# Performance work log

Hardware: AMD Instinct MI355X
Metric: run time of the kernel (lower is better)

## Reference

```python
import jax, jax.numpy as jnp
import numpy as np

N_GRAPHS = 2048
NODES_PER_GRAPH = 128
M = NODES_PER_GRAPH // 2  # atoms per monomer
N_NODES = N_GRAPHS * NODES_PER_GRAPH
DEG = 4
N_EDGES = N_NODES * DEG
F_IN = 64
D = 128
EPS = 1e-5
SLOPE = 0.01


def leaky(h):
    return jnp.where(h > 0, h, SLOPE * h)


def setup_inputs() -> dict:
    key = jax.random.key(0)
    ks = jax.random.split(key, 24)
    rng = np.random.default_rng(0)
    # intra-graph random edges, degree ~4
    offs = np.repeat(np.arange(N_GRAPHS, dtype=np.int32) * NODES_PER_GRAPH, NODES_PER_GRAPH * DEG)
    src = offs + rng.integers(0, NODES_PER_GRAPH, N_EDGES).astype(np.int32)
    dst = offs + rng.integers(0, NODES_PER_GRAPH, N_EDGES).astype(np.int32)
    edge_index = jnp.asarray(np.stack([src, dst]), dtype=jnp.int32)
    batch_index = jnp.asarray(np.repeat(np.arange(N_GRAPHS, dtype=np.int32), NODES_PER_GRAPH))
    # first half of each graph = monomer A (weight 0.3), second half = monomer B (0.7)
    mw_graph = np.concatenate([np.full(M, 0.3, np.float32), np.full(M, 0.7, np.float32)])
    monomer_weight = jnp.asarray(np.tile(mw_graph, N_GRAPHS)[:, None])
    s = 0.05
    inp = {
        "x": jax.random.normal(ks[0], (N_NODES, F_IN), jnp.float32),
        "monomer_weight": monomer_weight,
        "Wc0s": jax.random.normal(ks[1], (F_IN, D)) * s,
        "Wc0n": jax.random.normal(ks[2], (F_IN, D)) * s,
        "bc0": jnp.zeros((D,)),
        "g0": jnp.ones((D,)), "b0": jnp.zeros((D,)),
        "m0": jax.random.normal(ks[3], (D,)) * s, "v0": jnp.ones((D,)),
        "Wc1s": jax.random.normal(ks[4], (D, D)) * s,
        "Wc1n": jax.random.normal(ks[5], (D, D)) * s,
        "bc1": jnp.zeros((D,)),
        "g1": jnp.ones((D,)), "b1": jnp.zeros((D,)),
        "m1": jax.random.normal(ks[6], (D,)) * s, "v1": jnp.ones((D,)),
        "Wa": jax.random.normal(ks[7], (D, D)) * s, "ba": jnp.zeros((D,)),
        "Wr0": jax.random.normal(ks[8], (D, D)) * s, "br0": jnp.zeros((D,)),
        "Wr1": jax.random.normal(ks[9], (D, D)) * s, "br1": jnp.zeros((D,)),
        "Wout": jax.random.normal(ks[10], (D, 1)) * s, "bout": jnp.zeros((1,)),
        "edge_index": edge_index,
        "batch_index": batch_index,
    }
    return inp


def reference(x, monomer_weight, Wc0s, Wc0n, bc0, g0, b0, m0, v0,
              Wc1s, Wc1n, bc1, g1, b1, m1, v1, Wa, ba,
              Wr0, br0, Wr1, br1, Wout, bout, edge_index, batch_index):
    src, dst = edge_index[0], edge_index[1]
    n = x.shape[0]
    deg = jnp.clip(jax.ops.segment_sum(jnp.ones_like(src, jnp.float32), dst, num_segments=n), 1.0)

    def conv(h, Ws, Wn, b):
        agg = jax.ops.segment_sum(h[src], dst, num_segments=n) / deg[:, None]
        return h @ Ws + agg @ Wn + b

    def bn(h, g, b, rm, rv):
        return (h - rm) * jax.lax.rsqrt(rv + EPS) * g + b

    # conv + BN(eval) + leaky_relu (+ dropout identity in eval)
    h = leaky(bn(conv(x, Wc0s, Wc0n, bc0), g0, b0, m0, v0))
    h = leaky(bn(conv(h, Wc1s, Wc1n, bc1), g1, b1, m1, v1))
    # apply monomer weighting BeforePooling
    h = h * monomer_weight
    # pairwise monomer cross-attention (regular layout: [G, 2M, D])
    hg = h.reshape(N_GRAPHS, NODES_PER_GRAPH, D)
    mA, mB = hg[:, :M], hg[:, M:]
    pA = leaky(mA @ Wa + ba)
    pB = leaky(mB @ Wa + ba)
    pair = jax.nn.sigmoid(jnp.einsum('gmd,gnd->gmn', pA, pB))
    newA = jnp.einsum('gmn,gnd->gmd', pair, pB) + mA
    newB = jnp.einsum('gmn,gmd->gnd', pair, pA) + mB
    h = jnp.concatenate([newA, newB], axis=1).reshape(n, D)
    # scatter-based global mean pool
    pooled = jax.ops.segment_sum(h, batch_index, num_segments=N_GRAPHS)
    cnt = jax.ops.segment_sum(jnp.ones((n,), jnp.float32), batch_index, num_segments=N_GRAPHS)
    pooled = pooled / cnt[:, None]
    # readout MLP (dropout identity in eval)
    r = leaky(pooled @ Wr0 + br0)
    r = leaky(r @ Wr1 + br1)
    return r @ Wout + bout
```

## Files before the change

kernel.cpp:

```cpp
#include <hip/hip_runtime.h>

#define N_EDGES_C 1048576

typedef __attribute__((ext_vector_type(8))) __bf16 bf16x8;
typedef __attribute__((ext_vector_type(4))) __bf16 bf16x4;
typedef __attribute__((ext_vector_type(4))) float f32x4;
typedef __attribute__((ext_vector_type(4))) unsigned int u32x4;

#define MFMA16(a,b,c) __builtin_amdgcn_mfma_f32_16x16x32_bf16((a),(b),(c),0,0,0)

__device__ __forceinline__ unsigned short f2bf(float f) {
  unsigned int u = __builtin_bit_cast(unsigned int, f);
  u = (u + 0x7fffu + ((u >> 16) & 1u)) >> 16;
  return (unsigned short)u;
}
__device__ __forceinline__ float bf2f(unsigned short h) {
  unsigned int u = ((unsigned int)h) << 16;
  return __builtin_bit_cast(float, u);
}

__device__ __forceinline__ bf16x8 fragM(const unsigned short* sM, int row, int kb, int lane) {
  int r = row + (lane & 15);
  int cb = (kb + ((lane >> 4) << 3)) * 2;
  return *(const bf16x8*)((const char*)sM + r * 256 + (cb ^ ((r & 7) << 4)));
}
__device__ __forceinline__ void putBf(unsigned short* sM, int r, int c, float v) {
  *(__bf16*)((char*)sM + r * 256 + ((c * 2) ^ ((r & 7) << 4))) = (__bf16)v;
}
__device__ __forceinline__ bf16x8 adjFrag(const unsigned char* sCc, float inv,
                                          int mBase, int kb, int lane) {
  int m = mBase + (lane & 15);
  int c = (kb + ((lane >> 4) << 3)) ^ ((m & 7) << 3);
  const unsigned int* p = (const unsigned int*)(sCc + m * 128 + c);
  unsigned int w0 = p[0], w1 = p[1];
  bf16x8 r;
#pragma unroll
  for (int i = 0; i < 4; i++) {
    r[i]     = (__bf16)((float)((w0 >> (8 * i)) & 0xffu) * inv);
    r[4 + i] = (__bf16)((float)((w1 >> (8 * i)) & 0xffu) * inv);
  }
  return r;
}

__device__ __forceinline__ u32x4 stG32(const unsigned short* src, int KS, int ko, int t) {
  int row = t >> 2, ks = t & 3;
  return *(const u32x4*)(src + row * KS + ko + ks * 8);
}
__device__ __forceinline__ void stW32(unsigned short* buf, int t, u32x4 v) {
  int row = t >> 2, ks = t & 3;
  int slot = (ks + row + (row >> 2)) & 3;
  *(u32x4*)((char*)buf + row * 64 + slot * 16) = v;
}
__device__ __forceinline__ bf16x8 fragW32(const unsigned short* buf, int nc, int lane) {
  int r = nc + (lane & 15);
  int ks = lane >> 4;
  int slot = (ks + r + (r >> 2)) & 3;
  return *(const bf16x8*)((const char*)buf + r * 64 + slot * 16);
}

__global__ void prep_kernel(const float* __restrict__ Wc0s, const float* __restrict__ Wc0n,
                            const float* __restrict__ Wc1s, const float* __restrict__ Wc1n,
                            const float* __restrict__ Wa,
                            const float* __restrict__ bc0, const float* __restrict__ g0,
                            const float* __restrict__ b0, const float* __restrict__ m0,
                            const float* __restrict__ v0,
                            const float* __restrict__ bc1, const float* __restrict__ g1,
                            const float* __restrict__ b1, const float* __restrict__ m1,
                            const float* __restrict__ v1,
                            const float* __restrict__ Wr0, const float* __restrict__ Wr1,
                            unsigned short* __restrict__ wbf, float* __restrict__ cst,
                            float* __restrict__ wr0t, float* __restrict__ wr1t) {
  int t = blockIdx.x * blockDim.x + threadIdx.x;
  if (t < 8192) {
    int d = t >> 6, f = t & 63;
    wbf[t]        = f2bf(Wc0s[f * 128 + d]);
    wbf[8192 + t] = f2bf(Wc0n[f * 128 + d]);
  } else if (t < 24576) {
    int i = t - 8192;
    int d = i >> 7, k = i & 127;
    wbf[16384 + i] = f2bf(Wc1s[k * 128 + d]);
    wbf[32768 + i] = f2bf(Wc1n[k * 128 + d]);
    wbf[49152 + i] = f2bf(Wa[k * 128 + d]);
  } else if (t < 24704) {
    int d = t - 24576;
    float s0 = g0[d] * rsqrtf(v0[d] + 1e-5f);
    cst[d]       = s0;
    cst[128 + d] = (bc0[d] - m0[d]) * s0 + b0[d];
    float s1 = g1[d] * rsqrtf(v1[d] + 1e-5f);
    cst[256 + d] = s1;
    cst[384 + d] = (bc1[d] - m1[d]) * s1 + b1[d];
  } else if (t < 57472) {
    int i = t - 24704;
    int which = i >> 14;
    int k = i & 16383;
    int d = k >> 7, j = k & 127;
    float v = (which ? Wr1 : Wr0)[j * 128 + d];
    (which ? wr1t : wr0t)[k] = v;
  }
}

__global__ __launch_bounds__(512, 4)
void gnn_fused(const float* __restrict__ x, const float* __restrict__ mwt,
               const int* __restrict__ ei,
               const unsigned short* __restrict__ wbf, const float* __restrict__ cst,
               const float* __restrict__ ba,
               const float* __restrict__ wr0t, const float* __restrict__ br0,
               const float* __restrict__ wr1t, const float* __restrict__ br1,
               const float* __restrict__ Wout, const float* __restrict__ bout,
               float* __restrict__ out) {
  __shared__ unsigned short sM[128 * 128];
  __shared__ unsigned char  sC[128 * 128];
  __shared__ unsigned short sW[3][4096];
  __shared__ float sInv[128];
  __shared__ float sPool[128];
  __shared__ float sV1[128];
  __shared__ float sOut;

  const int g = blockIdx.x;
  const int t = threadIdx.x;
  const int lane = t & 63;
  const int w = t >> 6;
  const int col = lane & 15;
  const int r0 = (lane >> 4) << 2;
  const f32x4 zero = {0.f, 0.f, 0.f, 0.f};
  u32x4 st0, st1;

  st0 = stG32(wbf + 8192, 64, 0, t);
  st1 = stG32(wbf + 8192, 64, 32, t);
  u32x4 st2 = stG32(wbf, 64, 0, t);
  {
    unsigned int* c32 = (unsigned int*)sC;
    for (int i = t; i < 4096; i += 512) c32[i] = 0u;
    if (t < 128) { sPool[t] = 0.f; sV1[t] = 0.f; }
    if (t == 0) sOut = 0.f;
  }
  {
    const float4* xg = (const float4*)(x + (size_t)g * 8192);
#pragma unroll
    for (int i = 0; i < 4; i++) {
      int vi = t + i * 512;
      float4 v = xg[vi];
      int node = vi >> 4;
      int f = (vi & 15) * 4;
      bf16x4 q = {(__bf16)v.x, (__bf16)v.y, (__bf16)v.z, (__bf16)v.w};
      *(bf16x4*)((char*)sM + node * 256 + ((f * 2) ^ ((node & 7) << 4))) = q;
    }
  }
  __syncthreads();

  {
    int e = g * 512 + t;
    int ls_ = ei[e] & 127;
    int ld_ = ei[N_EDGES_C + e] & 127;
    int cb = ls_ ^ ((ld_ & 7) << 3);
    int idx = ld_ * 128 + cb;
    atomicAdd((unsigned int*)(sC + (idx & ~3)), 1u << ((idx & 3) * 8));
  }
  stW32(sW[0], t, st0);
  stW32(sW[1], t, st1);
  stW32(sW[2], t, st2);
  bf16x8 xA0 = fragM(sM, w * 16, 0, lane);
  bf16x8 xA1 = fragM(sM, w * 16, 32, lane);
  __syncthreads();

  f32x4 acc[8];

  {
    int row = t >> 2, q = t & 3;
    const unsigned int* rp = (const unsigned int*)(sC + row * 128) + q * 8;
    int ssum = 0;
#pragma unroll
    for (int i = 0; i < 8; i++) {
      unsigned int v = rp[i];
      ssum += (int)(v & 0xff) + (int)((v >> 8) & 0xff) + (int)((v >> 16) & 0xff) + (int)(v >> 24);
    }
    ssum += __shfl_xor(ssum, 1);
    ssum += __shfl_xor(ssum, 2);
    if (q == 0) sInv[row] = 1.f / (float)(ssum > 1 ? ssum : 1);
  }
  st0 = stG32(wbf, 64, 32, t);
  st1 = stG32(wbf + 32768, 128, 0, t);
#pragma unroll
  for (int n = 0; n < 8; n++) acc[n] = zero;
#pragma unroll
  for (int n = 0; n < 8; n++) acc[n] = MFMA16(xA0, fragW32(sW[0], n * 16, lane), acc[n]);
#pragma unroll
  for (int n = 0; n < 8; n++) acc[n] = MFMA16(xA1, fragW32(sW[1], n * 16, lane), acc[n]);
#pragma unroll
  for (int n = 0; n < 8; n++) {
    bf16x4 q = {(__bf16)acc[n][0], (__bf16)acc[n][1], (__bf16)acc[n][2], (__bf16)acc[n][3]};
    int d = n * 16 + col;
    *(bf16x4*)((char*)sM + d * 256 + (((w * 16 + r0) * 2) ^ ((d & 7) << 4))) = q;
  }
  __syncthreads();

  stW32(sW[0], t, st0);
  stW32(sW[1], t, st1);
  st0 = stG32(wbf + 32768, 128, 32, t);
  const float invRow = sInv[w * 16 + col];
#pragma unroll
  for (int n = 0; n < 8; n++) acc[n] = zero;
#pragma unroll
  for (int n = 0; n < 8; n++) acc[n] = MFMA16(xA0, fragW32(sW[2], n * 16, lane), acc[n]);
  for (int kb = 0; kb < 4; kb++) {
    bf16x8 aF = adjFrag(sC, invRow, w * 16, kb * 32, lane);
#pragma unroll
    for (int n = 0; n < 8; n++)
      acc[n] = MFMA16(aF, fragM(sM, n * 16, kb * 32, lane), acc[n]);
  }
  __syncthreads();

  stW32(sW[2], t, st0);
  st1 = stG32(wbf + 32768, 128, 64, t);
#pragma unroll
  for (int n = 0; n < 8; n++) acc[n] = MFMA16(xA1, fragW32(sW[0], n * 16, lane), acc[n]);
#pragma unroll
  for (int n = 0; n < 8; n++) {
    int d = n * 16 + col;
    float mul = cst[d], add = cst[128 + d];
#pragma unroll
    for (int r = 0; r < 4; r++) {
      float v = acc[n][r] * mul + add;
      v = v > 0.f ? v : 0.01f * v;
      putBf(sM, w * 16 + r0 + r, d, v);
    }
  }
  bf16x8 hA0 = fragM(sM, w * 16, 0, lane);
  bf16x8 hA1 = fragM(sM, w * 16, 32, lane);
  bf16x8 hA2 = fragM(sM, w * 16, 64, lane);
  bf16x8 hA3 = fragM(sM, w * 16, 96, lane);
  __syncthreads();

  stW32(sW[0], t, st1);
  st0 = stG32(wbf + 32768, 128, 96, t);
#pragma unroll
  for (int n = 0; n < 8; n++) acc[n] = zero;
#pragma unroll
  for (int n = 0; n < 8; n++) acc[n] = MFMA16(hA0, fragW32(sW[1], n * 16, lane), acc[n]);
  __syncthreads();

  stW32(sW[1], t, st0);
  st1 = stG32(wbf + 16384, 128, 0, t);
#pragma unroll
  for (int n = 0; n < 8; n++) acc[n] = MFMA16(hA1, fragW32(sW[2], n * 16, lane), acc[n]);
  __syncthreads();

  stW32(sW[2], t, st1);
  st0 = stG32(wbf + 16384, 128, 32, t);
#pragma unroll
  for (int n = 0; n < 8; n++) acc[n] = MFMA16(hA2, fragW32(sW[0], n * 16, lane), acc[n]);
  __syncthreads();

  stW32(sW[0], t, st0);
  st1 = stG32(wbf + 16384, 128, 64, t);
#pragma unroll
  for (int n = 0; n < 8; n++) acc[n] = MFMA16(hA3, fragW32(sW[1], n * 16, lane), acc[n]);
#pragma unroll
  for (int n = 0; n < 8; n++) {
    bf16x4 q = {(__bf16)acc[n][0], (__bf16)acc[n][1], (__bf16)acc[n][2], (__bf16)acc[n][3]};
    int d = n * 16 + col;
    *(bf16x4*)((char*)sM + d * 256 + (((w * 16 + r0) * 2) ^ ((d & 7) << 4))) = q;
  }
  __syncthreads();

  stW32(sW[1], t, st1);
  st0 = stG32(wbf + 16384, 128, 96, t);
#pragma unroll
  for (int n = 0; n < 8; n++) acc[n] = zero;
  for (int kb = 0; kb < 4; kb++) {
    bf16x8 aF = adjFrag(sC, invRow, w * 16, kb * 32, lane);
#pragma unroll
    for (int n = 0; n < 8; n++)
      acc[n] = MFMA16(aF, fragM(sM, n * 16, kb * 32, lane), acc[n]);
  }
  __syncthreads();

  st1 = stG32(wbf + 49152, 128, 0, t);
#pragma unroll
  for (int n = 0; n < 8; n++) acc[n] = MFMA16(hA0, fragW32(sW[2], n * 16, lane), acc[n]);
  __syncthreads();

  stW32(sW[2], t, st0);
  st0 = stG32(wbf + 49152, 128, 32, t);
  float mwr[4];
#pragma unroll
  for (int r = 0; r < 4; r++) mwr[r] = mwt[(size_t)g * 128 + w * 16 + r0 + r];
#pragma unroll
  for (int n = 0; n < 8; n++) acc[n] = MFMA16(hA1, fragW32(sW[0], n * 16, lane), acc[n]);
  __syncthreads();

  stW32(sW[0], t, st1);
  st1 = stG32(wbf + 49152, 128, 64, t);
#pragma unroll
  for (int n = 0; n < 8; n++) acc[n] = MFMA16(hA2, fragW32(sW[1], n * 16, lane), acc[n]);
  __syncthreads();

  stW32(sW[1], t, st0);
  st0 = stG32(wbf + 49152, 128, 96, t);
#pragma unroll
  for (int n = 0; n < 8; n++) acc[n] = MFMA16(hA3, fragW32(sW[2], n * 16, lane), acc[n]);
#pragma unroll
  for (int n = 0; n < 8; n++) {
    int d = n * 16 + col;
    float mul = cst[256 + d], add = cst[384 + d];
    float csum = 0.f;
#pragma unroll
    for (int r = 0; r < 4; r++) {
      float v = acc[n][r] * mul + add;
      v = v > 0.f ? v : 0.01f * v;
      v *= mwr[r];
      putBf(sM, w * 16 + r0 + r, d, v);
      csum += v;
    }
    csum += __shfl_xor(csum, 16);
    csum += __shfl_xor(csum, 32);
    if (lane < 16) atomicAdd(&sPool[d], csum);
  }
  hA0 = fragM(sM, w * 16, 0, lane);
  hA1 = fragM(sM, w * 16, 32, lane);
  hA2 = fragM(sM, w * 16, 64, lane);
  hA3 = fragM(sM, w * 16, 96, lane);
  __syncthreads();

  stW32(sW[2], t, st1);
#pragma unroll
  for (int n = 0; n < 8; n++) acc[n] = zero;
#pragma unroll
  for (int n = 0; n < 8; n++) acc[n] = MFMA16(hA0, fragW32(sW[0], n * 16, lane), acc[n]);
  __syncthreads();

  stW32(sW[0], t, st0);
#pragma unroll
  for (int n = 0; n < 8; n++) acc[n] = MFMA16(hA1, fragW32(sW[1], n * 16, lane), acc[n]);
  __syncthreads();

#pragma unroll
  for (int n = 0; n < 8; n++) acc[n] = MFMA16(hA2, fragW32(sW[2], n * 16, lane), acc[n]);
  __syncthreads();

#pragma unroll
  for (int n = 0; n < 8; n++) acc[n] = MFMA16(hA3, fragW32(sW[0], n * 16, lane), acc[n]);
#pragma unroll
  for (int n = 0; n < 8; n++) {
    int d = n * 16 + col;
    float bav = ba[d];
#pragma unroll
    for (int r = 0; r < 4; r++) {
      float v = acc[n][r] + bav;
      v = v > 0.f ? v : 0.01f * v;
      putBf(sM, w * 16 + r0 + r, d, v);
    }
  }
  __syncthreads();

  {
    f32x4 acc2[2] = {zero, zero};
    for (int kb = 0; kb < 128; kb += 32) {
#pragma unroll
      for (int i = 0; i < 2; i++) {
        int T = w * 2 + i;
        bf16x8 a = fragM(sM, (T >> 2) * 16, kb, lane);
        bf16x8 b = fragM(sM, 64 + (T & 3) * 16, kb, lane);
        acc2[i] = MFMA16(a, b, acc2[i]);
      }
    }
#pragma unroll
    for (int i = 0; i < 2; i++) {
      int T = w * 2 + i, mb = (T >> 2) * 16, nb = (T & 3) * 16;
      float s0 = 1.f / (1.f + __expf(-acc2[i][0]));
      float s1 = 1.f / (1.f + __expf(-acc2[i][1]));
      float s2 = 1.f / (1.f + __expf(-acc2[i][2]));
      float s3 = 1.f / (1.f + __expf(-acc2[i][3]));
      atomicAdd(&sV1[64 + nb + col], s0 + s1 + s2 + s3);
#pragma unroll
      for (int m = 1; m < 16; m <<= 1) {
        s0 += __shfl_xor(s0, m);
        s1 += __shfl_xor(s1, m);
        s2 += __shfl_xor(s2, m);
        s3 += __shfl_xor(s3, m);
      }
      if (col < 4) {
        float v = col == 0 ? s0 : (col == 1 ? s1 : (col == 2 ? s2 : s3));
        atomicAdd(&sV1[mb + r0 + col], v);
      }
    }
  }
  __syncthreads();

  {
    int d = t & 127, q = t >> 7;
    float s = 0.f;
#pragma unroll
    for (int i = 0; i < 32; i++) {
      int node = q * 32 + i;
      float u = sV1[node];
      float pv = bf2f(*(const unsigned short*)((const char*)sM + node * 256 +
                                               ((2 * d) ^ ((node & 7) << 4))));
      s += u * pv;
    }
    atomicAdd(&sPool[d], s);
  }
  __syncthreads();

  if (t < 128) sPool[t] *= (1.f / 128.f);
  __syncthreads();
  {
    int d = t >> 2, q = t & 3;
    const float* row = wr0t + d * 128 + q * 32;
    float s = 0.f;
#pragma unroll
    for (int j = 0; j < 32; j++) s += sPool[q * 32 + j] * row[j];
    s += __shfl_xor(s, 1);
    s += __shfl_xor(s, 2);
    if (q == 0) { s += br0[d]; sV1[d] = s > 0.f ? s : 0.01f * s; }
  }
  __syncthreads();
  {
    int d = t >> 2, q = t & 3;
    const float* row = wr1t + d * 128 + q * 32;
    float s = 0.f;
#pragma unroll
    for (int j = 0; j < 32; j++) s += sV1[q * 32 + j] * row[j];
    s += __shfl_xor(s, 1);
    s += __shfl_xor(s, 2);
    if (q == 0) { s += br1[d]; sPool[d] = s > 0.f ? s : 0.01f * s; }
  }
  __syncthreads();
  if (t < 128) atomicAdd(&sOut, sPool[t] * Wout[t]);
  __syncthreads();
  if (t == 0) out[g] = sOut + bout[0];
}

extern "C" void kernel_launch(void* const* d_in, const int* in_sizes, int n_in,
                              void* d_out, int out_size, void* d_ws, size_t ws_size,
                              hipStream_t stream) {
  const float* x     = (const float*)d_in[0];
  const float* mwt   = (const float*)d_in[1];
  const float* Wc0s  = (const float*)d_in[2];
  const float* Wc0n  = (const float*)d_in[3];
  const float* bc0   = (const float*)d_in[4];
  const float* g0    = (const float*)d_in[5];
  const float* b0    = (const float*)d_in[6];
  const float* m0    = (const float*)d_in[7];
  const float* v0    = (const float*)d_in[8];
  const float* Wc1s  = (const float*)d_in[9];
  const float* Wc1n  = (const float*)d_in[10];
  const float* bc1   = (const float*)d_in[11];
  const float* g1    = (const float*)d_in[12];
  const float* b1    = (const float*)d_in[13];
  const float* m1    = (const float*)d_in[14];
  const float* v1    = (const float*)d_in[15];
  const float* Wa    = (const float*)d_in[16];
  const float* ba    = (const float*)d_in[17];
  const float* Wr0   = (const float*)d_in[18];
  const float* br0   = (const float*)d_in[19];
  const float* Wr1   = (const float*)d_in[20];
  const float* br1   = (const float*)d_in[21];
  const float* Wout  = (const float*)d_in[22];
  const float* bout  = (const float*)d_in[23];
  const int*   ei    = (const int*)d_in[24];

  unsigned short* wbf = (unsigned short*)d_ws;
  float* cst  = (float*)((char*)d_ws + 131072);
  float* wr0t = (float*)((char*)d_ws + 133120);
  float* wr1t = (float*)((char*)d_ws + 198656);

  prep_kernel<<<dim3(225), dim3(256), 0, stream>>>(Wc0s, Wc0n, Wc1s, Wc1n, Wa,
                                                   bc0, g0, b0, m0, v0,
                                                   bc1, g1, b1, m1, v1,
                                                   Wr0, Wr1, wbf, cst, wr0t, wr1t);
  gnn_fused<<<dim3(2048), dim3(512), 0, stream>>>(x, mwt, ei, wbf, cst, ba,
                                                  wr0t, br0, wr1t, br1, Wout, bout,
                                                  (float*)d_out);
}
```

Measured before the change: 161.5 us.

## Use LDS-only barriers, compute degree by atomics, split readout MLP into separate kernel

Every __syncthreads is replaced with a barrier that waits only on LDS counters (lgkmcnt), so global weight prefetches stay in flight across barriers. Edge indices are loaded earlier to overlap with the x load. Node degree is now accumulated with float atomics at edge-insert time, which removes the row-sum pass over the count matrix. The readout MLP moves out of the fused kernel into a second 128-thread kernel that reads pooled vectors from workspace. This adds a launch and a global round trip for the pooled data, and the custom barrier relies on vmcnt ordering being handled elsewhere.

```diff
diff --git a/kernel.cpp b/kernel.cpp
--- a/kernel.cpp
+++ b/kernel.cpp
@@ -8,6 +8,10 @@
 typedef __attribute__((ext_vector_type(4))) unsigned int u32x4;
 
 #define MFMA16(a,b,c) __builtin_amdgcn_mfma_f32_16x16x32_bf16((a),(b),(c),0,0,0)
+
+#define BARRIER() do { asm volatile("s_waitcnt lgkmcnt(0)" ::: "memory"); \
+                       __builtin_amdgcn_s_barrier(); \
+                       asm volatile("" ::: "memory"); } while (0)
 
 __device__ __forceinline__ unsigned short f2bf(float f) {
   unsigned int u = __builtin_bit_cast(unsigned int, f);
@@ -104,19 +108,15 @@
                const int* __restrict__ ei,
                const unsigned short* __restrict__ wbf, const float* __restrict__ cst,
                const float* __restrict__ ba,
-               const float* __restrict__ wr0t, const float* __restrict__ br0,
-               const float* __restrict__ wr1t, const float* __restrict__ br1,
-               const float* __restrict__ Wout, const float* __restrict__ bout,
-               float* __restrict__ out) {
+               float* __restrict__ pooled) {
   __shared__ unsigned short sM[128 * 128];
   __shared__ unsigned char  sC[128 * 128];
   __shared__ unsigned short sW[3][4096];
-  __shared__ float sInv[128];
+  __shared__ float sDeg[128];
   __shared__ float sPool[128];
   __shared__ float sV1[128];
-  __shared__ float sOut;
-
-  const int g = blockIdx.x;
+
+  const int gb = blockIdx.x;
   const int t = threadIdx.x;
   const int lane = t & 63;
   const int w = t >> 6;
@@ -128,14 +128,19 @@
   st0 = stG32(wbf + 8192, 64, 0, t);
   st1 = stG32(wbf + 8192, 64, 32, t);
   u32x4 st2 = stG32(wbf, 64, 0, t);
+  int els, eld;
+  {
+    int e = gb * 512 + t;
+    els = ei[e] & 127;
+    eld = ei[N_EDGES_C + e] & 127;
+  }
   {
     unsigned int* c32 = (unsigned int*)sC;
     for (int i = t; i < 4096; i += 512) c32[i] = 0u;
-    if (t < 128) { sPool[t] = 0.f; sV1[t] = 0.f; }
-    if (t == 0) sOut = 0.f;
-  }
-  {
-    const float4* xg = (const float4*)(x + (size_t)g * 8192);
+    if (t < 128) { sPool[t] = 0.f; sV1[t] = 0.f; sDeg[t] = 0.f; }
+  }
+  {
+    const float4* xg = (const float4*)(x + (size_t)gb * 8192);
 #pragma unroll
     for (int i = 0; i < 4; i++) {
       int vi = t + i * 512;
@@ -146,38 +151,23 @@
       *(bf16x4*)((char*)sM + node * 256 + ((f * 2) ^ ((node & 7) << 4))) = q;
     }
   }
-  __syncthreads();
-
-  {
-    int e = g * 512 + t;
-    int ls_ = ei[e] & 127;
-    int ld_ = ei[N_EDGES_C + e] & 127;
-    int cb = ls_ ^ ((ld_ & 7) << 3);
-    int idx = ld_ * 128 + cb;
+  BARRIER();
+
+  {
+    int cb = els ^ ((eld & 7) << 3);
+    int idx = eld * 128 + cb;
     atomicAdd((unsigned int*)(sC + (idx & ~3)), 1u << ((idx & 3) * 8));
+    atomicAdd(&sDeg[eld], 1.f);
   }
   stW32(sW[0], t, st0);
   stW32(sW[1], t, st1);
   stW32(sW[2], t, st2);
   bf16x8 xA0 = fragM(sM, w * 16, 0, lane);
   bf16x8 xA1 = fragM(sM, w * 16, 32, lane);
-  __syncthreads();
+  BARRIER();
 
   f32x4 acc[8];
 
-  {
-    int row = t >> 2, q = t & 3;
-    const unsigned int* rp = (const unsigned int*)(sC + row * 128) + q * 8;
-    int ssum = 0;
-#pragma unroll
-    for (int i = 0; i < 8; i++) {
-      unsigned int v = rp[i];
-      ssum += (int)(v & 0xff) + (int)((v >> 8) & 0xff) + (int)((v >> 16) & 0xff) + (int)(v >> 24);
-    }
-    ssum += __shfl_xor(ssum, 1);
-    ssum += __shfl_xor(ssum, 2);
-    if (q == 0) sInv[row] = 1.f / (float)(ssum > 1 ? ssum : 1);
-  }
   st0 = stG32(wbf, 64, 32, t);
   st1 = stG32(wbf + 32768, 128, 0, t);
 #pragma unroll
@@ -192,12 +182,12 @@
     int d = n * 16 + col;
     *(bf16x4*)((char*)sM + d * 256 + (((w * 16 + r0) * 2) ^ ((d & 7) << 4))) = q;
   }
-  __syncthreads();
+  BARRIER();
 
   stW32(sW[0], t, st0);
   stW32(sW[1], t, st1);
   st0 = stG32(wbf + 32768, 128, 32, t);
-  const float invRow = sInv[w * 16 + col];
+  const float invRow = 1.f / fmaxf(sDeg[w * 16 + col], 1.f);
 #pragma unroll
   for (int n = 0; n < 8; n++) acc[n] = zero;
 #pragma unroll
@@ -208,7 +198,7 @@
     for (int n = 0; n < 8; n++)
       acc[n] = MFMA16(aF, fragM(sM, n * 16, kb * 32, lane), acc[n]);
   }
-  __syncthreads();
+  BARRIER();
 
   stW32(sW[2], t, st0);
   st1 = stG32(wbf + 32768, 128, 64, t);
@@ -229,7 +219,7 @@
   bf16x8 hA1 = fragM(sM, w * 16, 32, lane);
   bf16x8 hA2 = fragM(sM, w * 16, 64, lane);
   bf16x8 hA3 = fragM(sM, w * 16, 96, lane);
-  __syncthreads();
+  BARRIER();
 
   stW32(sW[0], t, st1);
   st0 = stG32(wbf + 32768, 128, 96, t);
@@ -237,19 +227,19 @@
   for (int n = 0; n < 8; n++) acc[n] = zero;
 #pragma unroll
   for (int n = 0; n < 8; n++) acc[n] = MFMA16(hA0, fragW32(sW[1], n * 16, lane), acc[n]);
-  __syncthreads();
+  BARRIER();
 
   stW32(sW[1], t, st0);
   st1 = stG32(wbf + 16384, 128, 0, t);
 #pragma unroll
   for (int n = 0; n < 8; n++) acc[n] = MFMA16(hA1, fragW32(sW[2], n * 16, lane), acc[n]);
-  __syncthreads();
+  BARRIER();
 
   stW32(sW[2], t, st1);
   st0 = stG32(wbf + 16384, 128, 32, t);
 #pragma unroll
   for (int n = 0; n < 8; n++) acc[n] = MFMA16(hA2, fragW32(sW[0], n * 16, lane), acc[n]);
-  __syncthreads();
+  BARRIER();
 
   stW32(sW[0], t, st0);
   st1 = stG32(wbf + 16384, 128, 64, t);
@@ -261,7 +251,7 @@
     int d = n * 16 + col;
     *(bf16x4*)((char*)sM + d * 256 + (((w * 16 + r0) * 2) ^ ((d & 7) << 4))) = q;
   }
-  __syncthreads();
+  BARRIER();
 
   stW32(sW[1], t, st1);
   st0 = stG32(wbf + 16384, 128, 96, t);
@@ -273,27 +263,27 @@
     for (int n = 0; n < 8; n++)
       acc[n] = MFMA16(aF, fragM(sM, n * 16, kb * 32, lane), acc[n]);
   }
-  __syncthreads();
+  BARRIER();
 
   st1 = stG32(wbf + 49152, 128, 0, t);
 #pragma unroll
   for (int n = 0; n < 8; n++) acc[n] = MFMA16(hA0, fragW32(sW[2], n * 16, lane), acc[n]);
-  __syncthreads();
+  BARRIER();
 
   stW32(sW[2], t, st0);
   st0 = stG32(wbf + 49152, 128, 32, t);
   float mwr[4];
 #pragma unroll
-  for (int r = 0; r < 4; r++) mwr[r] = mwt[(size_t)g * 128 + w * 16 + r0 + r];
+  for (int r = 0; r < 4; r++) mwr[r] = mwt[(size_t)gb * 128 + w * 16 + r0 + r];
 #pragma unroll
   for (int n = 0; n < 8; n++) acc[n] = MFMA16(hA1, fragW32(sW[0], n * 16, lane), acc[n]);
-  __syncthreads();
+  BARRIER();
 
   stW32(sW[0], t, st1);
   st1 = stG32(wbf + 49152, 128, 64, t);
 #pragma unroll
   for (int n = 0; n < 8; n++) acc[n] = MFMA16(hA2, fragW32(sW[1], n * 16, lane), acc[n]);
-  __syncthreads();
+  BARRIER();
 
   stW32(sW[1], t, st0);
   st0 = stG32(wbf + 49152, 128, 96, t);
@@ -320,23 +310,23 @@
   hA1 = fragM(sM, w * 16, 32, lane);
   hA2 = fragM(sM, w * 16, 64, lane);
   hA3 = fragM(sM, w * 16, 96, lane);
-  __syncthreads();
+  BARRIER();
 
   stW32(sW[2], t, st1);
 #pragma unroll
   for (int n = 0; n < 8; n++) acc[n] = zero;
 #pragma unroll
   for (int n = 0; n < 8; n++) acc[n] = MFMA16(hA0, fragW32(sW[0], n * 16, lane), acc[n]);
-  __syncthreads();
+  BARRIER();
 
   stW32(sW[0], t, st0);
 #pragma unroll
   for (int n = 0; n < 8; n++) acc[n] = MFMA16(hA1, fragW32(sW[1], n * 16, lane), acc[n]);
-  __syncthreads();
+  BARRIER();
 
 #pragma unroll
   for (int n = 0; n < 8; n++) acc[n] = MFMA16(hA2, fragW32(sW[2], n * 16, lane), acc[n]);
-  __syncthreads();
+  BARRIER();
 
 #pragma unroll
   for (int n = 0; n < 8; n++) acc[n] = MFMA16(hA3, fragW32(sW[0], n * 16, lane), acc[n]);
@@ -351,7 +341,7 @@
       putBf(sM, w * 16 + r0 + r, d, v);
     }
   }
-  __syncthreads();
+  BARRIER();
 
   {
     f32x4 acc2[2] = {zero, zero};
@@ -385,7 +375,7 @@
       }
     }
   }
-  __syncthreads();
+  BARRIER();
 
   {
     int d = t & 127, q = t >> 7;
@@ -400,35 +390,46 @@
     }
     atomicAdd(&sPool[d], s);
   }
+  BARRIER();
+
+  if (t < 128) pooled[(size_t)gb * 128 + t] = sPool[t] * (1.f / 128.f);
+}
+
+__global__ __launch_bounds__(128)
+void readout_kernel(const float* __restrict__ pooled,
+                    const float* __restrict__ wr0t, const float* __restrict__ br0,
+                    const float* __restrict__ wr1t, const float* __restrict__ br1,
+                    const float* __restrict__ Wout, const float* __restrict__ bout,
+                    float* __restrict__ out) {
+  __shared__ float pl[128], t1[128];
+  __shared__ float sred[2];
+  int g = blockIdx.x, t = threadIdx.x;
+  pl[t] = pooled[(size_t)g * 128 + t];
   __syncthreads();
-
-  if (t < 128) sPool[t] *= (1.f / 128.f);
+  {
+    const float* row = wr0t + t * 128;
+    float s = 0.f;
+#pragma unroll 8
+    for (int j = 0; j < 128; j++) s += pl[j] * row[j];
+    s += br0[t];
+    t1[t] = s > 0.f ? s : 0.01f * s;
+  }
   __syncthreads();
-  {
-    int d = t >> 2, q = t & 3;
-    const float* row = wr0t + d * 128 + q * 32;
+  float v2;
+  {
+    const float* row = wr1t + t * 128;
     float s = 0.f;
-#pragma unroll
-    for (int j = 0; j < 32; j++) s += sPool[q * 32 + j] * row[j];
-    s += __shfl_xor(s, 1);
-    s += __shfl_xor(s, 2);
-    if (q == 0) { s += br0[d]; sV1[d] = s > 0.f ? s : 0.01f * s; }
-  }
+#pragma unroll 8
+    for (int j = 0; j < 128; j++) s += t1[j] * row[j];
+    s += br1[t];
+    s = s > 0.f ? s : 0.01f * s;
+    v2 = s * Wout[t];
+  }
+#pragma unroll
+  for (int m = 1; m < 64; m <<= 1) v2 += __shfl_xor(v2, m);
+  if ((t & 63) == 0) sred[t >> 6] = v2;
   __syncthreads();
-  {
-    int d = t >> 2, q = t & 3;
-    const float* row = wr1t + d * 128 + q * 32;
-    float s = 0.f;
-#pragma unroll
-    for (int j = 0; j < 32; j++) s += sV1[q * 32 + j] * row[j];
-    s += __shfl_xor(s, 1);
-    s += __shfl_xor(s, 2);
-    if (q == 0) { s += br1[d]; sPool[d] = s > 0.f ? s : 0.01f * s; }
-  }
-  __syncthreads();
-  if (t < 128) atomicAdd(&sOut, sPool[t] * Wout[t]);
-  __syncthreads();
-  if (t == 0) out[g] = sOut + bout[0];
+  if (t == 0) out[g] = sred[0] + sred[1] + bout[0];
 }
 
 extern "C" void kernel_launch(void* const* d_in, const int* in_sizes, int n_in,
@@ -461,15 +462,16 @@
   const int*   ei    = (const int*)d_in[24];
 
   unsigned short* wbf = (unsigned short*)d_ws;
-  float* cst  = (float*)((char*)d_ws + 131072);
-  float* wr0t = (float*)((char*)d_ws + 133120);
-  float* wr1t = (float*)((char*)d_ws + 198656);
+  float* cst    = (float*)((char*)d_ws + 131072);
+  float* wr0t   = (float*)((char*)d_ws + 133120);
+  float* wr1t   = (float*)((char*)d_ws + 198656);
+  float* pooled = (float*)((char*)d_ws + 264192);
 
   prep_kernel<<<dim3(225), dim3(256), 0, stream>>>(Wc0s, Wc0n, Wc1s, Wc1n, Wa,
                                                    bc0, g0, b0, m0, v0,
                                                    bc1, g1, b1, m1, v1,
                                                    Wr0, Wr1, wbf, cst, wr0t, wr1t);
-  gnn_fused<<<dim3(2048), dim3(512), 0, stream>>>(x, mwt, ei, wbf, cst, ba,
-                                                  wr0t, br0, wr1t, br1, Wout, bout,
-                                                  (float*)d_out);
-}
+  gnn_fused<<<dim3(2048), dim3(512), 0, stream>>>(x, mwt, ei, wbf, cst, ba, pooled);
+  readout_kernel<<<dim3(2048), dim3(128), 0, stream>>>(pooled, wr0t, br0, wr1t, br1,
+                                                       Wout, bout, (float*)d_out);
+}
```

Result: no change. 163.2 us (+1.0%).
